# Kernel tuning notes

Measured on AMD Instinct MI355X. Metric: run time of the kernel, lower is better.

Reference implementation:

```python
import jax, jax.numpy as jnp
import numpy as np

B, D, M, P, I, O = 256, 10, 32, 36, 8, 16
NUM_ITERATIONS = 3
EPS = 1e-07


def squash(s, axis=-1):
    sq = jnp.sum(s * s, axis=axis, keepdims=True)
    safe_norm = jnp.sqrt(sq + EPS)
    scale = sq / (1.0 + sq)
    return scale * (s / safe_norm)


def setup_inputs() -> dict:
    key = jax.random.key(0)
    kx, kw = jax.random.split(key)
    x = jax.random.normal(kx, (B, M, P, I), dtype=jnp.float32)
    # Parameter shape matches torch: [1, D, M, 1, O, I]
    W = 0.01 * jax.random.normal(kw, (1, D, M, 1, O, I), dtype=jnp.float32)
    return {"x": x, "W": W}


def reference(x, W):
    Wd = W[0, :, :, 0]  # [D, M, O, I]
    # u_hat: [B, D, M, P, O]
    u_hat = jnp.einsum('dmoi,bmpi->bdmpo', Wd, x)
    tu = jax.lax.stop_gradient(u_hat)
    b = jnp.zeros(u_hat.shape[:4], dtype=u_hat.dtype)  # [B, D, M, P]
    for _ in range(NUM_ITERATIONS - 1):
        c = jax.nn.softmax(b, axis=1)                 # over digit caps
        s = jnp.einsum('bdmp,bdmpo->bdo', c, tu)
        v = squash(s)
        b = b + jnp.einsum('bdmpo,bdo->bdmp', tu, v)
    # Final softmax over dim=3 (primary-cap axis), faithful to source
    c = jax.nn.softmax(b, axis=3)
    s = jnp.einsum('bdmp,bdmpo->bdo', c, u_hat)
    return squash(s)
```

## Files before the change

kernel.cpp:

```cpp
#include <hip/hip_runtime.h>
#include <math.h>

#define BB 256
#define DD 10
#define MM 32
#define PP 36
#define PH (PP/2)
#define II 8
#define OO 16
#define NT 640
#define XS 292
#define RS 37

__device__ __forceinline__ float dot8(const float4 a0, const float4 a1,
                                      const float4 b0, const float4 b1) {
    return a0.x*b0.x + a0.y*b0.y + a0.z*b0.z + a0.w*b0.w
         + a1.x*b1.x + a1.y*b1.y + a1.z*b1.z + a1.w*b1.w;
}

__global__ void __launch_bounds__(NT, 3) caps_routing(
    const float* __restrict__ x,
    const float* __restrict__ W,
    float* __restrict__ out)
{
    const int bidx = blockIdx.x;
    const int tid  = threadIdx.x;
    const int wave = tid >> 6;
    const int lane = tid & 63;
    const float* __restrict__ xb = x + (size_t)bidx * (MM*PP*II);

    __shared__ __align__(16) float xs  [MM*XS];
    __shared__ __align__(16) float z   [DD*MM*II];
    __shared__ __align__(16) float y   [DD*MM*II];
    __shared__ __align__(16) float ybar[MM*II];
    __shared__ __align__(16) float rinv[MM*RS];
    __shared__ __align__(16) float v_l [DD*OO];

    {
        const float4* xg = (const float4*)xb;
        #pragma unroll
        for (int k = 0; k < 4; ++k) {
            const int t = tid + k*NT;
            if (t < MM*72) {
                const int m = t / 72, r = t - m*72;
                *(float4*)(xs + m*XS + 4*r) = xg[t];
            }
        }
        if (tid < MM*II) {
            const int m = tid >> 3, i = tid & 7;
            const float* xr = xb + m*(PP*II) + i;
            float acc = 0.f;
            #pragma unroll 6
            for (int p = 0; p < PP; ++p) acc += xr[p*II];
            ybar[tid] = 0.1f * acc;
        }
    }
    __syncthreads();

    {
        const int d = wave;
        const int o = lane & 15, qq = lane >> 4;
        float s1 = 0.f;
        #pragma unroll
        for (int j = 0; j < 8; ++j) {
            const int m = qq*8 + j;
            const float4* wp = (const float4*)(W + ((size_t)((d*MM + m)*OO + o)) * II);
            const float4* yp = (const float4*)(ybar + m*II);
            s1 += dot8(wp[0], wp[1], yp[0], yp[1]);
        }
        s1 += __shfl_xor(s1, 16, 64);
        s1 += __shfl_xor(s1, 32, 64);
        float sq = s1 * s1;
        sq += __shfl_xor(sq, 1, 64);
        sq += __shfl_xor(sq, 2, 64);
        sq += __shfl_xor(sq, 4, 64);
        sq += __shfl_xor(sq, 8, 64);
        const float v1 = (sq / (1.f + sq)) * (s1 / sqrtf(sq + 1e-7f));
        if (lane < OO) v_l[d*OO + lane] = v1;

        const float4 vv0 = *(const float4*)(v_l + d*OO);
        const float4 vv1 = *(const float4*)(v_l + d*OO + 4);
        const float4 vv2 = *(const float4*)(v_l + d*OO + 8);
        const float4 vv3 = *(const float4*)(v_l + d*OO + 12);
        const float vs[16] = {vv0.x,vv0.y,vv0.z,vv0.w, vv1.x,vv1.y,vv1.z,vv1.w,
                              vv2.x,vv2.y,vv2.z,vv2.w, vv3.x,vv3.y,vv3.z,vv3.w};
        const int mz = lane >> 1, ihz = lane & 1;
        const float* wz = W + ((size_t)(d*MM + mz)*OO) * II + ihz*4;
        float a0 = 0.f, a1 = 0.f, a2 = 0.f, a3 = 0.f;
        #pragma unroll
        for (int o2 = 0; o2 < OO; ++o2) {
            const float4 wv = *(const float4*)(wz + o2*II);
            a0 += wv.x * vs[o2]; a1 += wv.y * vs[o2];
            a2 += wv.z * vs[o2]; a3 += wv.w * vs[o2];
        }
        *(float4*)(z + (d*MM + mz)*II + ihz*4) = make_float4(a0, a1, a2, a3);
    }
    __syncthreads();

    #pragma unroll
    for (int k = 0; k < 2; ++k) {
        const int t = tid + k*NT;
        if (t < MM*PP) {
            const int m = t / PP, p = t - m*PP;
            const float4* xp = (const float4*)(xs + m*XS + p*II);
            const float4 x0 = xp[0], x1 = xp[1];
            float se = 0.f;
            #pragma unroll
            for (int d2 = 0; d2 < DD; ++d2) {
                const float4* zp = (const float4*)(z + (d2*MM + m)*II);
                se += __expf(dot8(x0, x1, zp[0], zp[1]));
            }
            rinv[m*RS + p] = 1.0f / se;
        }
    }
    __syncthreads();

    {
        const int d = wave;
        const float* __restrict__ zd = z + d*(MM*II);
        float* __restrict__ yd = y + d*(MM*II);

        const int mF = lane & 31;
        const int ph = lane >> 5;
        const float* xr = xs + mF*XS + (ph*PH)*II;
        const float4 zf0 = *(const float4*)(zd + mF*II);
        const float4 zf1 = *(const float4*)(zd + mF*II + 4);

        {
            const float* rr = rinv + mF*RS + ph*PH;
            float a0=0.f,a1=0.f,a2=0.f,a3=0.f,a4=0.f,a5=0.f,a6=0.f,a7=0.f;
            #pragma unroll 6
            for (int q = 0; q < PH; ++q) {
                const float4 x0 = *(const float4*)(xr + q*II);
                const float4 x1 = *(const float4*)(xr + q*II + 4);
                const float e = __expf(dot8(x0, x1, zf0, zf1)) * rr[q];
                a0 += e*x0.x; a1 += e*x0.y; a2 += e*x0.z; a3 += e*x0.w;
                a4 += e*x1.x; a5 += e*x1.y; a6 += e*x1.z; a7 += e*x1.w;
            }
            a0 += __shfl_xor(a0, 32, 64); a1 += __shfl_xor(a1, 32, 64);
            a2 += __shfl_xor(a2, 32, 64); a3 += __shfl_xor(a3, 32, 64);
            a4 += __shfl_xor(a4, 32, 64); a5 += __shfl_xor(a5, 32, 64);
            a6 += __shfl_xor(a6, 32, 64); a7 += __shfl_xor(a7, 32, 64);
            const float4 wv = ph ? make_float4(a4,a5,a6,a7) : make_float4(a0,a1,a2,a3);
            *(float4*)(yd + mF*II + ph*4) = wv;
        }

        const int o = lane & 15, qq = lane >> 4;
        float s2 = 0.f;
        #pragma unroll
        for (int j = 0; j < 8; ++j) {
            const int m = qq*8 + j;
            const float4* wp = (const float4*)(W + ((size_t)((d*MM + m)*OO + o)) * II);
            const float4* yp = (const float4*)(yd + m*II);
            s2 += dot8(wp[0], wp[1], yp[0], yp[1]);
        }
        s2 += __shfl_xor(s2, 16, 64);
        s2 += __shfl_xor(s2, 32, 64);
        float sq = s2 * s2;
        sq += __shfl_xor(sq, 1, 64);
        sq += __shfl_xor(sq, 2, 64);
        sq += __shfl_xor(sq, 4, 64);
        sq += __shfl_xor(sq, 8, 64);
        const float v2 = (sq / (1.f + sq)) * (s2 / sqrtf(sq + 1e-7f));
        if (lane < OO) v_l[d*OO + lane] = v2;
        const float4 vv0 = *(const float4*)(v_l + d*OO);
        const float4 vv1 = *(const float4*)(v_l + d*OO + 4);
        const float4 vv2 = *(const float4*)(v_l + d*OO + 8);
        const float4 vv3 = *(const float4*)(v_l + d*OO + 12);
        const float vs[16] = {vv0.x,vv0.y,vv0.z,vv0.w, vv1.x,vv1.y,vv1.z,vv1.w,
                              vv2.x,vv2.y,vv2.z,vv2.w, vv3.x,vv3.y,vv3.z,vv3.w};

        float4 zf20, zf21;
        {
            const float* wz = W + ((size_t)(d*MM + mF)*OO) * II;
            float b0=0.f,b1=0.f,b2=0.f,b3=0.f,b4=0.f,b5=0.f,b6=0.f,b7=0.f;
            #pragma unroll
            for (int j = 0; j < 8; ++j) {
                const int o2 = ph*8 + j;
                const float4 w0 = *(const float4*)(wz + o2*II);
                const float4 w1 = *(const float4*)(wz + o2*II + 4);
                const float s = vs[o2];
                b0 += w0.x*s; b1 += w0.y*s; b2 += w0.z*s; b3 += w0.w*s;
                b4 += w1.x*s; b5 += w1.y*s; b6 += w1.z*s; b7 += w1.w*s;
            }
            b0 += __shfl_xor(b0, 32, 64); b1 += __shfl_xor(b1, 32, 64);
            b2 += __shfl_xor(b2, 32, 64); b3 += __shfl_xor(b3, 32, 64);
            b4 += __shfl_xor(b4, 32, 64); b5 += __shfl_xor(b5, 32, 64);
            b6 += __shfl_xor(b6, 32, 64); b7 += __shfl_xor(b7, 32, 64);
            zf20 = make_float4(zf0.x + b0, zf0.y + b1, zf0.z + b2, zf0.w + b3);
            zf21 = make_float4(zf1.x + b4, zf1.y + b5, zf1.z + b6, zf1.w + b7);
        }

        {
            float se = 0.f;
            float a0=0.f,a1=0.f,a2=0.f,a3=0.f,a4=0.f,a5=0.f,a6=0.f,a7=0.f;
            #pragma unroll 6
            for (int q = 0; q < PH; ++q) {
                const float4 x0 = *(const float4*)(xr + q*II);
                const float4 x1 = *(const float4*)(xr + q*II + 4);
                const float e = __expf(dot8(x0, x1, zf20, zf21));
                se += e;
                a0 += e*x0.x; a1 += e*x0.y; a2 += e*x0.z; a3 += e*x0.w;
                a4 += e*x1.x; a5 += e*x1.y; a6 += e*x1.z; a7 += e*x1.w;
            }
            se += __shfl_xor(se, 32, 64);
            a0 += __shfl_xor(a0, 32, 64); a1 += __shfl_xor(a1, 32, 64);
            a2 += __shfl_xor(a2, 32, 64); a3 += __shfl_xor(a3, 32, 64);
            a4 += __shfl_xor(a4, 32, 64); a5 += __shfl_xor(a5, 32, 64);
            a6 += __shfl_xor(a6, 32, 64); a7 += __shfl_xor(a7, 32, 64);
            const float rs = 1.f / se;
            const float4 wv = ph ? make_float4(a4*rs,a5*rs,a6*rs,a7*rs)
                                 : make_float4(a0*rs,a1*rs,a2*rs,a3*rs);
            *(float4*)(yd + mF*II + ph*4) = wv;
        }

        float s3 = 0.f;
        #pragma unroll
        for (int j = 0; j < 8; ++j) {
            const int m = qq*8 + j;
            const float4* wp = (const float4*)(W + ((size_t)((d*MM + m)*OO + o)) * II);
            const float4* yp = (const float4*)(yd + m*II);
            s3 += dot8(wp[0], wp[1], yp[0], yp[1]);
        }
        s3 += __shfl_xor(s3, 16, 64);
        s3 += __shfl_xor(s3, 32, 64);
        float sq3 = s3 * s3;
        sq3 += __shfl_xor(sq3, 1, 64);
        sq3 += __shfl_xor(sq3, 2, 64);
        sq3 += __shfl_xor(sq3, 4, 64);
        sq3 += __shfl_xor(sq3, 8, 64);
        const float r = (sq3 / (1.f + sq3)) * (s3 / sqrtf(sq3 + 1e-7f));
        if (lane < OO)
            out[(size_t)bidx * (DD*OO) + d*OO + o] = r;
    }
}

extern "C" void kernel_launch(void* const* d_in, const int* in_sizes, int n_in,
                              void* d_out, int out_size, void* d_ws, size_t ws_size,
                              hipStream_t stream) {
    (void)in_sizes; (void)n_in; (void)out_size; (void)d_ws; (void)ws_size;
    const float* x = (const float*)d_in[0];
    const float* W = (const float*)d_in[1];
    float* out = (float*)d_out;
    caps_routing<<<dim3(BB), dim3(NT), 0, stream>>>(x, W, out);
}
```

Before: 78.68 us.

## Split fused routing kernel into three kernels with per-digit tail blocks

Replaces the single per-batch kernel with three launches: a prework kernel that computes ybar, v1 and z1 into workspace, a kernel that computes the softmax-over-digits reciprocals across 512 blocks, and a tail kernel with one 64-thread block per (batch, digit) that runs the remaining routing from global memory. The aim is more parallelism and occupancy than 256 large blocks with heavy shared-memory use, and the block indices are remapped so that one batch's blocks share an XCD and its L2. The cost is two extra launches, global-memory round trips for z1 and rinv, and repeated reads of x from global or cache instead of shared memory.

```diff
diff --git a/kernel.cpp b/kernel.cpp
--- a/kernel.cpp
+++ b/kernel.cpp
@@ -5,12 +5,12 @@
 #define DD 10
 #define MM 32
 #define PP 36
-#define PH (PP/2)
+#define PH2 18
 #define II 8
 #define OO 16
-#define NT 640
-#define XS 292
-#define RS 37
+
+#define Z1_OFF   0
+#define RINV_OFF (BB*DD*MM*II)
 
 __device__ __forceinline__ float dot8(const float4 a0, const float4 a1,
                                       const float4 b0, const float4 b1) {
@@ -18,74 +18,57 @@
          + a1.x*b1.x + a1.y*b1.y + a1.z*b1.z + a1.w*b1.w;
 }
 
-__global__ void __launch_bounds__(NT, 3) caps_routing(
-    const float* __restrict__ x,
-    const float* __restrict__ W,
-    float* __restrict__ out)
+__global__ void __launch_bounds__(512, 1) k1_prework(
+    const float* __restrict__ x, const float* __restrict__ W,
+    float* __restrict__ ws)
 {
-    const int bidx = blockIdx.x;
-    const int tid  = threadIdx.x;
-    const int wave = tid >> 6;
-    const int lane = tid & 63;
-    const float* __restrict__ xb = x + (size_t)bidx * (MM*PP*II);
-
-    __shared__ __align__(16) float xs  [MM*XS];
-    __shared__ __align__(16) float z   [DD*MM*II];
-    __shared__ __align__(16) float y   [DD*MM*II];
+    const int b   = blockIdx.x;
+    const int tid = threadIdx.x;
+    const float* __restrict__ xb = x + (size_t)b * (MM*PP*II);
     __shared__ __align__(16) float ybar[MM*II];
-    __shared__ __align__(16) float rinv[MM*RS];
     __shared__ __align__(16) float v_l [DD*OO];
 
     {
-        const float4* xg = (const float4*)xb;
-        #pragma unroll
-        for (int k = 0; k < 4; ++k) {
-            const int t = tid + k*NT;
-            if (t < MM*72) {
-                const int m = t / 72, r = t - m*72;
-                *(float4*)(xs + m*XS + 4*r) = xg[t];
-            }
-        }
-        if (tid < MM*II) {
-            const int m = tid >> 3, i = tid & 7;
-            const float* xr = xb + m*(PP*II) + i;
-            float acc = 0.f;
-            #pragma unroll 6
-            for (int p = 0; p < PP; ++p) acc += xr[p*II];
-            ybar[tid] = 0.1f * acc;
-        }
+        const int m = tid >> 4, i = (tid >> 1) & 7, ph = tid & 1;
+        const float* xr = xb + (m*PP + ph*PH2)*II + i;
+        float acc = 0.f;
+        #pragma unroll
+        for (int q = 0; q < PH2; ++q) acc += xr[q*II];
+        acc += __shfl_xor(acc, 1, 64);
+        if (ph == 0) ybar[m*II + i] = 0.1f * acc;
     }
     __syncthreads();
 
-    {
-        const int d = wave;
-        const int o = lane & 15, qq = lane >> 4;
+    if (tid < DD*OO*2) {
+        const int d = tid >> 5, o = (tid >> 1) & 15, mh = tid & 1;
         float s1 = 0.f;
         #pragma unroll
-        for (int j = 0; j < 8; ++j) {
-            const int m = qq*8 + j;
+        for (int j = 0; j < 16; ++j) {
+            const int m = mh*16 + j;
             const float4* wp = (const float4*)(W + ((size_t)((d*MM + m)*OO + o)) * II);
             const float4* yp = (const float4*)(ybar + m*II);
             s1 += dot8(wp[0], wp[1], yp[0], yp[1]);
         }
-        s1 += __shfl_xor(s1, 16, 64);
-        s1 += __shfl_xor(s1, 32, 64);
+        s1 += __shfl_xor(s1, 1, 64);
         float sq = s1 * s1;
-        sq += __shfl_xor(sq, 1, 64);
         sq += __shfl_xor(sq, 2, 64);
         sq += __shfl_xor(sq, 4, 64);
         sq += __shfl_xor(sq, 8, 64);
-        const float v1 = (sq / (1.f + sq)) * (s1 / sqrtf(sq + 1e-7f));
-        if (lane < OO) v_l[d*OO + lane] = v1;
-
+        sq += __shfl_xor(sq, 16, 64);
+        v_l[d*OO + o] = (sq / (1.f + sq)) * (s1 / sqrtf(sq + 1e-7f));
+    }
+    __syncthreads();
+
+    float* __restrict__ z1 = ws + Z1_OFF + (size_t)b * (DD*MM*II);
+    for (int s = tid; s < DD*MM*2; s += 512) {
+        const int d = s >> 6, r = s & 63, mz = r >> 1, ih = r & 1;
         const float4 vv0 = *(const float4*)(v_l + d*OO);
         const float4 vv1 = *(const float4*)(v_l + d*OO + 4);
         const float4 vv2 = *(const float4*)(v_l + d*OO + 8);
         const float4 vv3 = *(const float4*)(v_l + d*OO + 12);
         const float vs[16] = {vv0.x,vv0.y,vv0.z,vv0.w, vv1.x,vv1.y,vv1.z,vv1.w,
                               vv2.x,vv2.y,vv2.z,vv2.w, vv3.x,vv3.y,vv3.z,vv3.w};
-        const int mz = lane >> 1, ihz = lane & 1;
-        const float* wz = W + ((size_t)(d*MM + mz)*OO) * II + ihz*4;
+        const float* wz = W + ((size_t)((d*MM + mz)*OO)) * II + ih*4;
         float a0 = 0.f, a1 = 0.f, a2 = 0.f, a3 = 0.f;
         #pragma unroll
         for (int o2 = 0; o2 < OO; ++o2) {
@@ -93,154 +76,169 @@
             a0 += wv.x * vs[o2]; a1 += wv.y * vs[o2];
             a2 += wv.z * vs[o2]; a3 += wv.w * vs[o2];
         }
-        *(float4*)(z + (d*MM + mz)*II + ihz*4) = make_float4(a0, a1, a2, a3);
-    }
-    __syncthreads();
-
+        *(float4*)(z1 + (d*MM + mz)*II + ih*4) = make_float4(a0, a1, a2, a3);
+    }
+}
+
+__global__ void __launch_bounds__(576) k2_rinv(
+    const float* __restrict__ x, const float* __restrict__ ws_in,
+    float* __restrict__ ws)
+{
+    const int q   = blockIdx.x;
+    const int xcd = q & 7, r = q >> 3;
+    const int ph  = r & 1, b = xcd + 8*(r >> 1);
+    const int t   = threadIdx.x;
+    const int m   = t / PH2, p = ph*PH2 + (t - (t/PH2)*PH2);
+
+    const float4* xp = (const float4*)(x + ((size_t)b*MM*PP + m*PP + p) * II);
+    const float4 x0 = xp[0], x1 = xp[1];
+    const float* __restrict__ z1 = ws_in + Z1_OFF + (size_t)b * (DD*MM*II);
+    float se = 0.f;
     #pragma unroll
-    for (int k = 0; k < 2; ++k) {
-        const int t = tid + k*NT;
-        if (t < MM*PP) {
-            const int m = t / PP, p = t - m*PP;
-            const float4* xp = (const float4*)(xs + m*XS + p*II);
-            const float4 x0 = xp[0], x1 = xp[1];
-            float se = 0.f;
-            #pragma unroll
-            for (int d2 = 0; d2 < DD; ++d2) {
-                const float4* zp = (const float4*)(z + (d2*MM + m)*II);
-                se += __expf(dot8(x0, x1, zp[0], zp[1]));
-            }
-            rinv[m*RS + p] = 1.0f / se;
-        }
-    }
-    __syncthreads();
-
-    {
-        const int d = wave;
-        const float* __restrict__ zd = z + d*(MM*II);
-        float* __restrict__ yd = y + d*(MM*II);
-
-        const int mF = lane & 31;
-        const int ph = lane >> 5;
-        const float* xr = xs + mF*XS + (ph*PH)*II;
-        const float4 zf0 = *(const float4*)(zd + mF*II);
-        const float4 zf1 = *(const float4*)(zd + mF*II + 4);
-
-        {
-            const float* rr = rinv + mF*RS + ph*PH;
-            float a0=0.f,a1=0.f,a2=0.f,a3=0.f,a4=0.f,a5=0.f,a6=0.f,a7=0.f;
-            #pragma unroll 6
-            for (int q = 0; q < PH; ++q) {
-                const float4 x0 = *(const float4*)(xr + q*II);
-                const float4 x1 = *(const float4*)(xr + q*II + 4);
-                const float e = __expf(dot8(x0, x1, zf0, zf1)) * rr[q];
-                a0 += e*x0.x; a1 += e*x0.y; a2 += e*x0.z; a3 += e*x0.w;
-                a4 += e*x1.x; a5 += e*x1.y; a6 += e*x1.z; a7 += e*x1.w;
-            }
-            a0 += __shfl_xor(a0, 32, 64); a1 += __shfl_xor(a1, 32, 64);
-            a2 += __shfl_xor(a2, 32, 64); a3 += __shfl_xor(a3, 32, 64);
-            a4 += __shfl_xor(a4, 32, 64); a5 += __shfl_xor(a5, 32, 64);
-            a6 += __shfl_xor(a6, 32, 64); a7 += __shfl_xor(a7, 32, 64);
-            const float4 wv = ph ? make_float4(a4,a5,a6,a7) : make_float4(a0,a1,a2,a3);
-            *(float4*)(yd + mF*II + ph*4) = wv;
-        }
-
-        const int o = lane & 15, qq = lane >> 4;
-        float s2 = 0.f;
+    for (int d = 0; d < DD; ++d) {
+        const float4* zp = (const float4*)(z1 + (d*MM + m)*II);
+        se += __expf(dot8(x0, x1, zp[0], zp[1]));
+    }
+    ws[RINV_OFF + (size_t)b*(PP*MM) + p*MM + m] = 1.0f / se;
+}
+
+__global__ void __launch_bounds__(64, 4) k3_tail(
+    const float* __restrict__ x, const float* __restrict__ W,
+    const float* __restrict__ ws, float* __restrict__ out)
+{
+    const int pb  = blockIdx.x;
+    const int xcd = pb & 7, idx = pb >> 3;
+    const int bq  = idx & 31, d = idx >> 5, b = xcd + 8*bq;
+    const int lane = threadIdx.x;
+
+    __shared__ __align__(16) float y  [MM*II];
+    __shared__ __align__(16) float v_l[OO];
+
+    const float* __restrict__ xb = x + (size_t)b * (MM*PP*II);
+    const float* __restrict__ z1 = ws + Z1_OFF + (size_t)b*(DD*MM*II) + d*(MM*II);
+    const float* __restrict__ ri = ws + RINV_OFF + (size_t)b*(PP*MM);
+
+    const int mF = lane & 31, ph = lane >> 5;
+    const float* xr = xb + (mF*PP + ph*PH2)*II;
+    const float4 zf0 = *(const float4*)(z1 + mF*II);
+    const float4 zf1 = *(const float4*)(z1 + mF*II + 4);
+
+    {
+        float a0=0.f,a1=0.f,a2=0.f,a3=0.f,a4=0.f,a5=0.f,a6=0.f,a7=0.f;
+        #pragma unroll
+        for (int qk = 0; qk < PH2; ++qk) {
+            const float4 x0 = *(const float4*)(xr + qk*II);
+            const float4 x1 = *(const float4*)(xr + qk*II + 4);
+            const float e = __expf(dot8(x0, x1, zf0, zf1)) * ri[(ph*PH2 + qk)*MM + mF];
+            a0 += e*x0.x; a1 += e*x0.y; a2 += e*x0.z; a3 += e*x0.w;
+            a4 += e*x1.x; a5 += e*x1.y; a6 += e*x1.z; a7 += e*x1.w;
+        }
+        a0 += __shfl_xor(a0, 32, 64); a1 += __shfl_xor(a1, 32, 64);
+        a2 += __shfl_xor(a2, 32, 64); a3 += __shfl_xor(a3, 32, 64);
+        a4 += __shfl_xor(a4, 32, 64); a5 += __shfl_xor(a5, 32, 64);
+        a6 += __shfl_xor(a6, 32, 64); a7 += __shfl_xor(a7, 32, 64);
+        const float4 wv = ph ? make_float4(a4,a5,a6,a7) : make_float4(a0,a1,a2,a3);
+        *(float4*)(y + mF*II + ph*4) = wv;
+    }
+
+    const int o = lane & 15, qq = lane >> 4;
+    float s2 = 0.f;
+    #pragma unroll
+    for (int j = 0; j < 8; ++j) {
+        const int m = qq*8 + j;
+        const float4* wp = (const float4*)(W + ((size_t)((d*MM + m)*OO + o)) * II);
+        const float4* yp = (const float4*)(y + m*II);
+        s2 += dot8(wp[0], wp[1], yp[0], yp[1]);
+    }
+    s2 += __shfl_xor(s2, 16, 64);
+    s2 += __shfl_xor(s2, 32, 64);
+    float sq = s2 * s2;
+    sq += __shfl_xor(sq, 1, 64);
+    sq += __shfl_xor(sq, 2, 64);
+    sq += __shfl_xor(sq, 4, 64);
+    sq += __shfl_xor(sq, 8, 64);
+    const float v2 = (sq / (1.f + sq)) * (s2 / sqrtf(sq + 1e-7f));
+    if (lane < OO) v_l[lane] = v2;
+    const float4 vv0 = *(const float4*)(v_l);
+    const float4 vv1 = *(const float4*)(v_l + 4);
+    const float4 vv2 = *(const float4*)(v_l + 8);
+    const float4 vv3 = *(const float4*)(v_l + 12);
+    const float vs[16] = {vv0.x,vv0.y,vv0.z,vv0.w, vv1.x,vv1.y,vv1.z,vv1.w,
+                          vv2.x,vv2.y,vv2.z,vv2.w, vv3.x,vv3.y,vv3.z,vv3.w};
+
+    float4 zf20, zf21;
+    {
+        const float* wz = W + ((size_t)(d*MM + mF)*OO) * II;
+        float b0=0.f,b1=0.f,b2=0.f,b3=0.f,b4=0.f,b5=0.f,b6=0.f,b7=0.f;
         #pragma unroll
         for (int j = 0; j < 8; ++j) {
-            const int m = qq*8 + j;
-            const float4* wp = (const float4*)(W + ((size_t)((d*MM + m)*OO + o)) * II);
-            const float4* yp = (const float4*)(yd + m*II);
-            s2 += dot8(wp[0], wp[1], yp[0], yp[1]);
-        }
-        s2 += __shfl_xor(s2, 16, 64);
-        s2 += __shfl_xor(s2, 32, 64);
-        float sq = s2 * s2;
-        sq += __shfl_xor(sq, 1, 64);
-        sq += __shfl_xor(sq, 2, 64);
-        sq += __shfl_xor(sq, 4, 64);
-        sq += __shfl_xor(sq, 8, 64);
-        const float v2 = (sq / (1.f + sq)) * (s2 / sqrtf(sq + 1e-7f));
-        if (lane < OO) v_l[d*OO + lane] = v2;
-        const float4 vv0 = *(const float4*)(v_l + d*OO);
-        const float4 vv1 = *(const float4*)(v_l + d*OO + 4);
-        const float4 vv2 = *(const float4*)(v_l + d*OO + 8);
-        const float4 vv3 = *(const float4*)(v_l + d*OO + 12);
-        const float vs[16] = {vv0.x,vv0.y,vv0.z,vv0.w, vv1.x,vv1.y,vv1.z,vv1.w,
-                              vv2.x,vv2.y,vv2.z,vv2.w, vv3.x,vv3.y,vv3.z,vv3.w};
-
-        float4 zf20, zf21;
-        {
-            const float* wz = W + ((size_t)(d*MM + mF)*OO) * II;
-            float b0=0.f,b1=0.f,b2=0.f,b3=0.f,b4=0.f,b5=0.f,b6=0.f,b7=0.f;
-            #pragma unroll
-            for (int j = 0; j < 8; ++j) {
-                const int o2 = ph*8 + j;
-                const float4 w0 = *(const float4*)(wz + o2*II);
-                const float4 w1 = *(const float4*)(wz + o2*II + 4);
-                const float s = vs[o2];
-                b0 += w0.x*s; b1 += w0.y*s; b2 += w0.z*s; b3 += w0.w*s;
-                b4 += w1.x*s; b5 += w1.y*s; b6 += w1.z*s; b7 += w1.w*s;
-            }
-            b0 += __shfl_xor(b0, 32, 64); b1 += __shfl_xor(b1, 32, 64);
-            b2 += __shfl_xor(b2, 32, 64); b3 += __shfl_xor(b3, 32, 64);
-            b4 += __shfl_xor(b4, 32, 64); b5 += __shfl_xor(b5, 32, 64);
-            b6 += __shfl_xor(b6, 32, 64); b7 += __shfl_xor(b7, 32, 64);
-            zf20 = make_float4(zf0.x + b0, zf0.y + b1, zf0.z + b2, zf0.w + b3);
-            zf21 = make_float4(zf1.x + b4, zf1.y + b5, zf1.z + b6, zf1.w + b7);
-        }
-
-        {
-            float se = 0.f;
-            float a0=0.f,a1=0.f,a2=0.f,a3=0.f,a4=0.f,a5=0.f,a6=0.f,a7=0.f;
-            #pragma unroll 6
-            for (int q = 0; q < PH; ++q) {
-                const float4 x0 = *(const float4*)(xr + q*II);
-                const float4 x1 = *(const float4*)(xr + q*II + 4);
-                const float e = __expf(dot8(x0, x1, zf20, zf21));
-                se += e;
-                a0 += e*x0.x; a1 += e*x0.y; a2 += e*x0.z; a3 += e*x0.w;
-                a4 += e*x1.x; a5 += e*x1.y; a6 += e*x1.z; a7 += e*x1.w;
-            }
-            se += __shfl_xor(se, 32, 64);
-            a0 += __shfl_xor(a0, 32, 64); a1 += __shfl_xor(a1, 32, 64);
-            a2 += __shfl_xor(a2, 32, 64); a3 += __shfl_xor(a3, 32, 64);
-            a4 += __shfl_xor(a4, 32, 64); a5 += __shfl_xor(a5, 32, 64);
-            a6 += __shfl_xor(a6, 32, 64); a7 += __shfl_xor(a7, 32, 64);
-            const float rs = 1.f / se;
-            const float4 wv = ph ? make_float4(a4*rs,a5*rs,a6*rs,a7*rs)
-                                 : make_float4(a0*rs,a1*rs,a2*rs,a3*rs);
-            *(float4*)(yd + mF*II + ph*4) = wv;
-        }
-
-        float s3 = 0.f;
-        #pragma unroll
-        for (int j = 0; j < 8; ++j) {
-            const int m = qq*8 + j;
-            const float4* wp = (const float4*)(W + ((size_t)((d*MM + m)*OO + o)) * II);
-            const float4* yp = (const float4*)(yd + m*II);
-            s3 += dot8(wp[0], wp[1], yp[0], yp[1]);
-        }
-        s3 += __shfl_xor(s3, 16, 64);
-        s3 += __shfl_xor(s3, 32, 64);
-        float sq3 = s3 * s3;
-        sq3 += __shfl_xor(sq3, 1, 64);
-        sq3 += __shfl_xor(sq3, 2, 64);
-        sq3 += __shfl_xor(sq3, 4, 64);
-        sq3 += __shfl_xor(sq3, 8, 64);
-        const float r = (sq3 / (1.f + sq3)) * (s3 / sqrtf(sq3 + 1e-7f));
-        if (lane < OO)
-            out[(size_t)bidx * (DD*OO) + d*OO + o] = r;
-    }
+            const int o2 = ph*8 + j;
+            const float4 w0 = *(const float4*)(wz + o2*II);
+            const float4 w1 = *(const float4*)(wz + o2*II + 4);
+            const float sv = vs[o2];
+            b0 += w0.x*sv; b1 += w0.y*sv; b2 += w0.z*sv; b3 += w0.w*sv;
+            b4 += w1.x*sv; b5 += w1.y*sv; b6 += w1.z*sv; b7 += w1.w*sv;
+        }
+        b0 += __shfl_xor(b0, 32, 64); b1 += __shfl_xor(b1, 32, 64);
+        b2 += __shfl_xor(b2, 32, 64); b3 += __shfl_xor(b3, 32, 64);
+        b4 += __shfl_xor(b4, 32, 64); b5 += __shfl_xor(b5, 32, 64);
+        b6 += __shfl_xor(b6, 32, 64); b7 += __shfl_xor(b7, 32, 64);
+        zf20 = make_float4(zf0.x + b0, zf0.y + b1, zf0.z + b2, zf0.w + b3);
+        zf21 = make_float4(zf1.x + b4, zf1.y + b5, zf1.z + b6, zf1.w + b7);
+    }
+
+    {
+        float se = 0.f;
+        float a0=0.f,a1=0.f,a2=0.f,a3=0.f,a4=0.f,a5=0.f,a6=0.f,a7=0.f;
+        #pragma unroll
+        for (int qk = 0; qk < PH2; ++qk) {
+            const float4 x0 = *(const float4*)(xr + qk*II);
+            const float4 x1 = *(const float4*)(xr + qk*II + 4);
+            const float e = __expf(dot8(x0, x1, zf20, zf21));
+            se += e;
+            a0 += e*x0.x; a1 += e*x0.y; a2 += e*x0.z; a3 += e*x0.w;
+            a4 += e*x1.x; a5 += e*x1.y; a6 += e*x1.z; a7 += e*x1.w;
+        }
+        se += __shfl_xor(se, 32, 64);
+        a0 += __shfl_xor(a0, 32, 64); a1 += __shfl_xor(a1, 32, 64);
+        a2 += __shfl_xor(a2, 32, 64); a3 += __shfl_xor(a3, 32, 64);
+        a4 += __shfl_xor(a4, 32, 64); a5 += __shfl_xor(a5, 32, 64);
+        a6 += __shfl_xor(a6, 32, 64); a7 += __shfl_xor(a7, 32, 64);
+        const float rs = 1.f / se;
+        const float4 wv = ph ? make_float4(a4*rs,a5*rs,a6*rs,a7*rs)
+                             : make_float4(a0*rs,a1*rs,a2*rs,a3*rs);
+        *(float4*)(y + mF*II + ph*4) = wv;
+    }
+
+    float s3 = 0.f;
+    #pragma unroll
+    for (int j = 0; j < 8; ++j) {
+        const int m = qq*8 + j;
+        const float4* wp = (const float4*)(W + ((size_t)((d*MM + m)*OO + o)) * II);
+        const float4* yp = (const float4*)(y + m*II);
+        s3 += dot8(wp[0], wp[1], yp[0], yp[1]);
+    }
+    s3 += __shfl_xor(s3, 16, 64);
+    s3 += __shfl_xor(s3, 32, 64);
+    float sq3 = s3 * s3;
+    sq3 += __shfl_xor(sq3, 1, 64);
+    sq3 += __shfl_xor(sq3, 2, 64);
+    sq3 += __shfl_xor(sq3, 4, 64);
+    sq3 += __shfl_xor(sq3, 8, 64);
+    const float r = (sq3 / (1.f + sq3)) * (s3 / sqrtf(sq3 + 1e-7f));
+    if (lane < OO)
+        out[((size_t)b*DD + d)*OO + o] = r;
 }
 
 extern "C" void kernel_launch(void* const* d_in, const int* in_sizes, int n_in,
                               void* d_out, int out_size, void* d_ws, size_t ws_size,
                               hipStream_t stream) {
-    (void)in_sizes; (void)n_in; (void)out_size; (void)d_ws; (void)ws_size;
+    (void)in_sizes; (void)n_in; (void)out_size; (void)ws_size;
     const float* x = (const float*)d_in[0];
     const float* W = (const float*)d_in[1];
     float* out = (float*)d_out;
-    caps_routing<<<dim3(BB), dim3(NT), 0, stream>>>(x, W, out);
-}
+    float* wsf = (float*)d_ws;
+    k1_prework<<<dim3(BB),     dim3(512), 0, stream>>>(x, W, wsf);
+    k2_rinv   <<<dim3(BB*2),   dim3(576), 0, stream>>>(x, wsf, wsf);
+    k3_tail   <<<dim3(BB*DD),  dim3(64),  0, stream>>>(x, W, wsf, out);
+}
```

Result: slower. 101.0 us (+28.4%).
